# Performance work log

Measured on AMD Instinct MI355X. Metric: run time of the kernel, lower is better.

## Reference

```python
import jax, jax.numpy as jnp
import numpy as np

B, T, C, HS = 256, 512, 64, 64

def setup_inputs() -> dict:
    key = jax.random.key(0)
    k1, k2, k3, k4 = jax.random.split(key, 4)
    x = jax.random.normal(k1, (B, T, C), dtype=jnp.float32)
    # store Linear weights as [in, out] so projection is x @ W
    w_key = jax.random.normal(k2, (C, HS), dtype=jnp.float32) * (C ** -0.5)
    w_query = jax.random.normal(k3, (C, HS), dtype=jnp.float32) * (C ** -0.5)
    w_value = jax.random.normal(k4, (C, HS), dtype=jnp.float32) * (C ** -0.5)
    return {"x": x, "w_key": w_key, "w_query": w_query, "w_value": w_value}

def reference(x, w_key, w_query, w_value):
    Bx, Tx, Cx = x.shape
    k = x @ w_key              # [B,T,HS]
    q = x @ w_query            # [B,T,HS]
    v = x @ w_value            # [B,T,HS]
    # NOTE: original scales by C**-0.5 (input channel dim), not head_size**-0.5
    wei = jnp.einsum("btd,bsd->bts", q, k) * (Cx ** -0.5)  # [B,T,T]
    causal = jnp.tril(jnp.ones((Tx, Tx), dtype=bool))
    wei = jnp.where(causal, wei, -jnp.inf)
    wei = jax.nn.softmax(wei, axis=-1)
    # dropout p=0.0 -> identity
    out = jnp.einsum("bts,bsd->btd", wei, v)  # [B,T,HS]
    return out
```

## Files before the change

kernel.cpp:

```cpp
#include <hip/hip_runtime.h>


#define SEQ 512
#define CH  64

#define SLOT_STRIDE 72
#define SLOT_SIZE   (32 * SLOT_STRIDE)
#define WOFF        (8 * SLOT_SIZE)

typedef __attribute__((ext_vector_type(8))) short bf16x8;
typedef __attribute__((ext_vector_type(4))) short bf16x4;
typedef __attribute__((ext_vector_type(4))) float f32x4;

static __device__ __forceinline__ short f2bf(float f) {
  union { float f; unsigned u; } v; v.f = f;
  unsigned r = v.u + 0x7FFFu + ((v.u >> 16) & 1u);
  return (short)(r >> 16);
}

static __device__ __forceinline__ bf16x4 pack4(f32x4 v) {
  bf16x4 r;
  r[0] = f2bf(v[0]); r[1] = f2bf(v[1]); r[2] = f2bf(v[2]); r[3] = f2bf(v[3]);
  return r;
}

static __device__ __forceinline__ f32x4 mfma32(bf16x8 a, bf16x8 b, f32x4 c) {
  return __builtin_amdgcn_mfma_f32_16x16x32_bf16(a, b, c, 0, 0, 0);
}

static __device__ __forceinline__ unsigned pperm(float hi, float lo) {
#if defined(__has_builtin) && __has_builtin(__builtin_amdgcn_perm)
  return __builtin_amdgcn_perm(__builtin_bit_cast(unsigned, hi),
                               __builtin_bit_cast(unsigned, lo), 0x07060302u);
#else
  return (__builtin_bit_cast(unsigned, hi) & 0xFFFF0000u) |
         (__builtin_bit_cast(unsigned, lo) >> 16);
#endif
}

#if defined(__has_builtin) && __has_builtin(__builtin_amdgcn_exp2f)
#define EXP2(v) __builtin_amdgcn_exp2f(v)
#else
#define EXP2(v) __expf((v) * 0.6931471805599453f)
#endif

static __device__ __forceinline__ void wave_lds_fence() {
  asm volatile("s_waitcnt lgkmcnt(0)" ::: "memory");
}

static __device__ __forceinline__ void make_qf(
    const float* __restrict__ xb, const bf16x8 WQf[4][2],
    unsigned short* slot, int q0, int l15, int quad, bf16x8 qf[2][2]) {
#pragma unroll
  for (int nn = 0; nn < 2; ++nn) {
    bf16x8 xa[2];
#pragma unroll
    for (int c = 0; c < 2; ++c) {
      const float* px = xb + (size_t)(q0 + nn * 16 + l15) * CH + c * 32 + quad * 8;
      float4 lo = *(const float4*)px;
      float4 hi = *(const float4*)(px + 4);
      bf16x8 f;
      f[0] = f2bf(lo.x); f[1] = f2bf(lo.y); f[2] = f2bf(lo.z); f[3] = f2bf(lo.w);
      f[4] = f2bf(hi.x); f[5] = f2bf(hi.y); f[6] = f2bf(hi.z); f[7] = f2bf(hi.w);
      xa[c] = f;
    }
#pragma unroll
    for (int cht = 0; cht < 4; ++cht) {
      f32x4 qt = {0.f, 0.f, 0.f, 0.f};
#pragma unroll
      for (int c = 0; c < 2; ++c)
        qt = mfma32(WQf[cht][c], xa[c], qt);
      *(bf16x4*)(slot + (nn * 16 + l15) * SLOT_STRIDE + cht * 16 + quad * 4) = pack4(qt);
    }
  }
  wave_lds_fence();
#pragma unroll
  for (int nn = 0; nn < 2; ++nn)
#pragma unroll
    for (int c = 0; c < 2; ++c)
      qf[nn][c] = *(const bf16x8*)(slot + (nn * 16 + l15) * SLOT_STRIDE + c * 32 + quad * 8);
  wave_lds_fence();
}

static __device__ __forceinline__ void run_strip(
    int s, const bf16x8 qf[2][2], const unsigned short* __restrict__ ldsK,
    const unsigned short* __restrict__ ldsV, float* __restrict__ outb,
    int lane, int l15, int quad) {
  const int q0 = s * 32;
  f32x4 ot[2][4];
#pragma unroll
  for (int nn = 0; nn < 2; ++nn)
#pragma unroll
    for (int cht = 0; cht < 4; ++cht) ot[nn][cht] = (f32x4){0.f, 0.f, 0.f, 0.f};
  float ls0 = 0.f, ls1 = 0.f;
  const int dthr = l15 - quad * 4;

  bf16x8 kf[4];
#pragma unroll
  for (int i = 0; i < 4; ++i)
    kf[i] = *(const bf16x8*)(ldsK + i * 512 + lane * 8);

#pragma unroll 1
  for (int kt = 0; kt <= s; ++kt) {
    const bool diag = (kt == s);
    bf16x8 vf[4];
    const unsigned short* vp = ldsV + kt * 2048;
#pragma unroll
    for (int i = 0; i < 4; ++i)
      vf[i] = *(const bf16x8*)(vp + i * 512 + lane * 8);
    bf16x8 kn[4];
    if (!diag) {
      const unsigned short* kp = ldsK + (kt + 1) * 2048;
#pragma unroll
      for (int i = 0; i < 4; ++i)
        kn[i] = *(const bf16x8*)(kp + i * 512 + lane * 8);
    }

    f32x4 st00 = {0.f,0.f,0.f,0.f}, st01 = {0.f,0.f,0.f,0.f};
    f32x4 st10 = {0.f,0.f,0.f,0.f}, st11 = {0.f,0.f,0.f,0.f};
    st00 = mfma32(kf[0], qf[0][0], st00); st00 = mfma32(kf[1], qf[0][1], st00);
    st01 = mfma32(kf[0], qf[1][0], st01); st01 = mfma32(kf[1], qf[1][1], st01);
    st11 = mfma32(kf[2], qf[1][0], st11); st11 = mfma32(kf[3], qf[1][1], st11);
    if (!diag) {
      st10 = mfma32(kf[2], qf[0][0], st10); st10 = mfma32(kf[3], qf[0][1], st10);
    }

    union { bf16x8 v; unsigned u[4]; } P0, P1;
    if (diag) {
#pragma unroll
      for (int r = 0; r < 4; ++r) {
        st00[r] = (r > dthr) ? 0.f : EXP2(st00[r]);  ls0 += st00[r];
        st11[r] = (r > dthr) ? 0.f : EXP2(st11[r]);  ls1 += st11[r];
        st01[r] = EXP2(st01[r]);                     ls1 += st01[r];
      }
      P0.u[0] = pperm(st00[1], st00[0]); P0.u[1] = pperm(st00[3], st00[2]);
      P0.u[2] = 0u;                      P0.u[3] = 0u;
      P1.u[0] = pperm(st01[1], st01[0]); P1.u[1] = pperm(st01[3], st01[2]);
      P1.u[2] = pperm(st11[1], st11[0]); P1.u[3] = pperm(st11[3], st11[2]);
    } else {
#pragma unroll
      for (int r = 0; r < 4; ++r) {
        st00[r] = EXP2(st00[r]);  ls0 += st00[r];
        st10[r] = EXP2(st10[r]);  ls0 += st10[r];
        st01[r] = EXP2(st01[r]);  ls1 += st01[r];
        st11[r] = EXP2(st11[r]);  ls1 += st11[r];
      }
      P0.u[0] = pperm(st00[1], st00[0]); P0.u[1] = pperm(st00[3], st00[2]);
      P0.u[2] = pperm(st10[1], st10[0]); P0.u[3] = pperm(st10[3], st10[2]);
      P1.u[0] = pperm(st01[1], st01[0]); P1.u[1] = pperm(st01[3], st01[2]);
      P1.u[2] = pperm(st11[1], st11[0]); P1.u[3] = pperm(st11[3], st11[2]);
    }

    ot[0][0] = mfma32(vf[0], P0.v, ot[0][0]);  ot[1][0] = mfma32(vf[0], P1.v, ot[1][0]);
    ot[0][1] = mfma32(vf[1], P0.v, ot[0][1]);  ot[1][1] = mfma32(vf[1], P1.v, ot[1][1]);
    ot[0][2] = mfma32(vf[2], P0.v, ot[0][2]);  ot[1][2] = mfma32(vf[2], P1.v, ot[1][2]);
    ot[0][3] = mfma32(vf[3], P0.v, ot[0][3]);  ot[1][3] = mfma32(vf[3], P1.v, ot[1][3]);

    if (!diag) {
#pragma unroll
      for (int i = 0; i < 4; ++i) kf[i] = kn[i];
    }
  }

  ls0 += __shfl_xor(ls0, 16); ls0 += __shfl_xor(ls0, 32);
  ls1 += __shfl_xor(ls1, 16); ls1 += __shfl_xor(ls1, 32);
  const float inv0 = 1.0f / ls0, inv1 = 1.0f / ls1;

#pragma unroll
  for (int nn = 0; nn < 2; ++nn) {
    const float inv = nn ? inv1 : inv0;
#pragma unroll
    for (int cht = 0; cht < 4; ++cht) {
      float4 v;
      v.x = ot[nn][cht][0] * inv; v.y = ot[nn][cht][1] * inv;
      v.z = ot[nn][cht][2] * inv; v.w = ot[nn][cht][3] * inv;
      *(float4*)(outb + (size_t)(q0 + nn * 16 + l15) * CH + cht * 16 + quad * 4) = v;
    }
  }
}

__global__ __launch_bounds__(512, 2)
void attn_fused(const float* __restrict__ x,
                const float* __restrict__ wk,
                const float* __restrict__ wq,
                const float* __restrict__ wv,
                float* __restrict__ out) {
  __shared__ alignas(16) unsigned short ldsK[SEQ * CH];
  __shared__ alignas(16) unsigned short ldsV[SEQ * CH];

  const int b    = blockIdx.x;
  const int w    = threadIdx.x >> 6;
  const int lane = threadIdx.x & 63;
  const int l15  = lane & 15;
  const int quad = lane >> 4;

  const float* xb   = x + (size_t)b * SEQ * CH;
  float*       outb = out + (size_t)b * SEQ * CH;

  {
    const int t = w >> 1, c = w & 1;
    const int k0 = c * 32 + quad * 8;
    const int n  = t * 16 + l15;
#pragma unroll
    for (int m = 0; m < 3; ++m) {
      const float* Wsrc  = (m == 0) ? wq : (m == 1) ? wk : wv;
      const float  scale = (m == 0) ? 0.18033688011112042f : 1.0f;
      bf16x8 fr;
#pragma unroll
      for (int j = 0; j < 8; ++j)
        fr[j] = f2bf(Wsrc[(k0 + j) * CH + n] * scale);
      *(bf16x8*)(ldsK + WOFF + (m * 8 + w) * 512 + lane * 8) = fr;
    }
  }
  __syncthreads();

  const int sA = w, sB = 15 - w;
  unsigned short* slot = ldsK + w * SLOT_SIZE;
  bf16x8 qfA[2][2], qfB[2][2];
  {
    bf16x8 WQf[4][2];
#pragma unroll
    for (int t = 0; t < 4; ++t)
#pragma unroll
      for (int c = 0; c < 2; ++c)
        WQf[t][c] = *(const bf16x8*)(ldsK + WOFF + (t * 2 + c) * 512 + lane * 8);
    make_qf(xb, WQf, slot, sA * 32, l15, quad, qfA);
    make_qf(xb, WQf, slot, sB * 32, l15, quad, qfB);
  }

  {
    bf16x8 WKf[4][2], WVf[4][2];
#pragma unroll
    for (int t = 0; t < 4; ++t)
#pragma unroll
      for (int c = 0; c < 2; ++c) {
        WKf[t][c] = *(const bf16x8*)(ldsK + WOFF + (8  + t * 2 + c) * 512 + lane * 8);
        WVf[t][c] = *(const bf16x8*)(ldsK + WOFF + (16 + t * 2 + c) * 512 + lane * 8);
      }
    __syncthreads();

#pragma unroll
    for (int sub = 0; sub < 4; ++sub) {
      const int t16 = w * 64 + sub * 16;
      bf16x8 xa[2];
#pragma unroll
      for (int c = 0; c < 2; ++c) {
        const float* px = xb + (size_t)(t16 + l15) * CH + c * 32 + quad * 8;
        float4 lo = *(const float4*)px;
        float4 hi = *(const float4*)(px + 4);
        bf16x8 f;
        f[0] = f2bf(lo.x); f[1] = f2bf(lo.y); f[2] = f2bf(lo.z); f[3] = f2bf(lo.w);
        f[4] = f2bf(hi.x); f[5] = f2bf(hi.y); f[6] = f2bf(hi.z); f[7] = f2bf(hi.w);
        xa[c] = f;
      }
#pragma unroll
      for (int cht = 0; cht < 4; ++cht) {
        f32x4 ak = {0.f, 0.f, 0.f, 0.f};
#pragma unroll
        for (int c = 0; c < 2; ++c)
          ak = mfma32(WKf[cht][c], xa[c], ak);
        const int cdst = cht >> 1;
        const int qp   = ((cht & 1) << 1) | (quad >> 1);
        *(bf16x4*)(ldsK + (t16 >> 4) * 1024 + cdst * 512 +
                   (qp * 16 + l15) * 8 + (quad & 1) * 4) = pack4(ak);
      }
#pragma unroll
      for (int nt = 0; nt < 4; ++nt) {
        f32x4 av = {0.f, 0.f, 0.f, 0.f};
#pragma unroll
        for (int c = 0; c < 2; ++c)
          av = mfma32(xa[c], WVf[nt][c], av);
        *(bf16x4*)(ldsV + (t16 >> 5) * 2048 + nt * 512 +
                   (quad * 16 + l15) * 8 + ((t16 >> 4) & 1) * 4) = pack4(av);
      }
    }
  }
  __syncthreads();

  run_strip(sA, qfA, ldsK, ldsV, outb, lane, l15, quad);
  run_strip(sB, qfB, ldsK, ldsV, outb, lane, l15, quad);
}

extern "C" void kernel_launch(void* const* d_in, const int* in_sizes, int n_in,
                              void* d_out, int out_size, void* d_ws, size_t ws_size,
                              hipStream_t stream) {
  const float* x  = (const float*)d_in[0];
  const float* wk = (const float*)d_in[1];
  const float* wq = (const float*)d_in[2];
  const float* wv = (const float*)d_in[3];
  (void)in_sizes; (void)n_in; (void)out_size; (void)d_ws; (void)ws_size;
  attn_fused<<<256, 512, 0, stream>>>(x, wk, wq, wv, (float*)d_out);
}
```

Baseline: 99.91 us.

## Split attention into 16-row query strips across 16 waves per block

Doubles the block to 1024 threads (16 waves). Each wave now handles two balanced 16-row query strips (s and 31-s) instead of two 32-row strips, and K/V projection work is split across more waves. This raises per-block parallelism and latency hiding, and halves per-wave register state (one output accumulator set). The cost is that each K/V tile is reloaded from LDS by twice as many waves per query row, and the diagonal handling becomes an odd/even partial tile. The weight-staging loop is reworked to distribute 24 fragments over 16 waves.

```diff
diff --git a/kernel.cpp b/kernel.cpp
--- a/kernel.cpp
+++ b/kernel.cpp
@@ -5,8 +5,8 @@
 #define CH  64
 
 #define SLOT_STRIDE 72
-#define SLOT_SIZE   (32 * SLOT_STRIDE)
-#define WOFF        (8 * SLOT_SIZE)
+#define SLOT_SIZE   (16 * SLOT_STRIDE)
+#define WOFF        (16 * SLOT_SIZE)
 
 typedef __attribute__((ext_vector_type(8))) short bf16x8;
 typedef __attribute__((ext_vector_type(4))) short bf16x4;
@@ -48,51 +48,46 @@
   asm volatile("s_waitcnt lgkmcnt(0)" ::: "memory");
 }
 
-static __device__ __forceinline__ void make_qf(
+static __device__ __forceinline__ void make_qf16(
     const float* __restrict__ xb, const bf16x8 WQf[4][2],
-    unsigned short* slot, int q0, int l15, int quad, bf16x8 qf[2][2]) {
-#pragma unroll
-  for (int nn = 0; nn < 2; ++nn) {
-    bf16x8 xa[2];
-#pragma unroll
-    for (int c = 0; c < 2; ++c) {
-      const float* px = xb + (size_t)(q0 + nn * 16 + l15) * CH + c * 32 + quad * 8;
-      float4 lo = *(const float4*)px;
-      float4 hi = *(const float4*)(px + 4);
-      bf16x8 f;
-      f[0] = f2bf(lo.x); f[1] = f2bf(lo.y); f[2] = f2bf(lo.z); f[3] = f2bf(lo.w);
-      f[4] = f2bf(hi.x); f[5] = f2bf(hi.y); f[6] = f2bf(hi.z); f[7] = f2bf(hi.w);
-      xa[c] = f;
-    }
-#pragma unroll
-    for (int cht = 0; cht < 4; ++cht) {
-      f32x4 qt = {0.f, 0.f, 0.f, 0.f};
-#pragma unroll
-      for (int c = 0; c < 2; ++c)
-        qt = mfma32(WQf[cht][c], xa[c], qt);
-      *(bf16x4*)(slot + (nn * 16 + l15) * SLOT_STRIDE + cht * 16 + quad * 4) = pack4(qt);
-    }
+    unsigned short* slot, int q0, int l15, int quad, bf16x8 qf[2]) {
+  bf16x8 xa[2];
+#pragma unroll
+  for (int c = 0; c < 2; ++c) {
+    const float* px = xb + (size_t)(q0 + l15) * CH + c * 32 + quad * 8;
+    float4 lo = *(const float4*)px;
+    float4 hi = *(const float4*)(px + 4);
+    bf16x8 f;
+    f[0] = f2bf(lo.x); f[1] = f2bf(lo.y); f[2] = f2bf(lo.z); f[3] = f2bf(lo.w);
+    f[4] = f2bf(hi.x); f[5] = f2bf(hi.y); f[6] = f2bf(hi.z); f[7] = f2bf(hi.w);
+    xa[c] = f;
+  }
+#pragma unroll
+  for (int cht = 0; cht < 4; ++cht) {
+    f32x4 qt = {0.f, 0.f, 0.f, 0.f};
+#pragma unroll
+    for (int c = 0; c < 2; ++c)
+      qt = mfma32(WQf[cht][c], xa[c], qt);
+    *(bf16x4*)(slot + l15 * SLOT_STRIDE + cht * 16 + quad * 4) = pack4(qt);
   }
   wave_lds_fence();
 #pragma unroll
-  for (int nn = 0; nn < 2; ++nn)
-#pragma unroll
-    for (int c = 0; c < 2; ++c)
-      qf[nn][c] = *(const bf16x8*)(slot + (nn * 16 + l15) * SLOT_STRIDE + c * 32 + quad * 8);
+  for (int c = 0; c < 2; ++c)
+    qf[c] = *(const bf16x8*)(slot + l15 * SLOT_STRIDE + c * 32 + quad * 8);
   wave_lds_fence();
 }
 
-static __device__ __forceinline__ void run_strip(
-    int s, const bf16x8 qf[2][2], const unsigned short* __restrict__ ldsK,
+static __device__ __forceinline__ void run_strip16(
+    int s, const bf16x8 qf[2], const unsigned short* __restrict__ ldsK,
     const unsigned short* __restrict__ ldsV, float* __restrict__ outb,
     int lane, int l15, int quad) {
-  const int q0 = s * 32;
-  f32x4 ot[2][4];
-#pragma unroll
-  for (int nn = 0; nn < 2; ++nn)
-#pragma unroll
-    for (int cht = 0; cht < 4; ++cht) ot[nn][cht] = (f32x4){0.f, 0.f, 0.f, 0.f};
-  float ls0 = 0.f, ls1 = 0.f;
+  const int q0  = s * 16;
+  const int nd  = s >> 1;
+  const int odd = s & 1;
+  f32x4 ot[4];
+#pragma unroll
+  for (int cht = 0; cht < 4; ++cht) ot[cht] = (f32x4){0.f, 0.f, 0.f, 0.f};
+  float ls = 0.f;
   const int dthr = l15 - quad * 4;
 
   bf16x8 kf[4];
@@ -101,85 +96,85 @@
     kf[i] = *(const bf16x8*)(ldsK + i * 512 + lane * 8);
 
 #pragma unroll 1
-  for (int kt = 0; kt <= s; ++kt) {
-    const bool diag = (kt == s);
+  for (int t = 0; t < nd; ++t) {
+    bf16x8 vf[4], kn[4];
+    const unsigned short* vp = ldsV + t * 2048;
+    const unsigned short* kp = ldsK + (t + 1) * 2048;
+#pragma unroll
+    for (int i = 0; i < 4; ++i) {
+      vf[i] = *(const bf16x8*)(vp + i * 512 + lane * 8);
+      kn[i] = *(const bf16x8*)(kp + i * 512 + lane * 8);
+    }
+
+    f32x4 s0 = {0.f,0.f,0.f,0.f}, s1 = {0.f,0.f,0.f,0.f};
+    s0 = mfma32(kf[0], qf[0], s0); s0 = mfma32(kf[1], qf[1], s0);
+    s1 = mfma32(kf[2], qf[0], s1); s1 = mfma32(kf[3], qf[1], s1);
+
+    union { bf16x8 v; unsigned u[4]; } P;
+#pragma unroll
+    for (int r = 0; r < 4; ++r) {
+      s0[r] = EXP2(s0[r]);  ls += s0[r];
+      s1[r] = EXP2(s1[r]);  ls += s1[r];
+    }
+    P.u[0] = pperm(s0[1], s0[0]); P.u[1] = pperm(s0[3], s0[2]);
+    P.u[2] = pperm(s1[1], s1[0]); P.u[3] = pperm(s1[3], s1[2]);
+
+    ot[0] = mfma32(vf[0], P.v, ot[0]);
+    ot[1] = mfma32(vf[1], P.v, ot[1]);
+    ot[2] = mfma32(vf[2], P.v, ot[2]);
+    ot[3] = mfma32(vf[3], P.v, ot[3]);
+
+#pragma unroll
+    for (int i = 0; i < 4; ++i) kf[i] = kn[i];
+  }
+
+  {
     bf16x8 vf[4];
-    const unsigned short* vp = ldsV + kt * 2048;
+    const unsigned short* vp = ldsV + (size_t)nd * 2048;
 #pragma unroll
     for (int i = 0; i < 4; ++i)
       vf[i] = *(const bf16x8*)(vp + i * 512 + lane * 8);
-    bf16x8 kn[4];
-    if (!diag) {
-      const unsigned short* kp = ldsK + (kt + 1) * 2048;
-#pragma unroll
-      for (int i = 0; i < 4; ++i)
-        kn[i] = *(const bf16x8*)(kp + i * 512 + lane * 8);
-    }
-
-    f32x4 st00 = {0.f,0.f,0.f,0.f}, st01 = {0.f,0.f,0.f,0.f};
-    f32x4 st10 = {0.f,0.f,0.f,0.f}, st11 = {0.f,0.f,0.f,0.f};
-    st00 = mfma32(kf[0], qf[0][0], st00); st00 = mfma32(kf[1], qf[0][1], st00);
-    st01 = mfma32(kf[0], qf[1][0], st01); st01 = mfma32(kf[1], qf[1][1], st01);
-    st11 = mfma32(kf[2], qf[1][0], st11); st11 = mfma32(kf[3], qf[1][1], st11);
-    if (!diag) {
-      st10 = mfma32(kf[2], qf[0][0], st10); st10 = mfma32(kf[3], qf[0][1], st10);
-    }
-
-    union { bf16x8 v; unsigned u[4]; } P0, P1;
-    if (diag) {
+
+    f32x4 s0 = {0.f,0.f,0.f,0.f}, s1 = {0.f,0.f,0.f,0.f};
+    s0 = mfma32(kf[0], qf[0], s0); s0 = mfma32(kf[1], qf[1], s0);
+    if (odd) { s1 = mfma32(kf[2], qf[0], s1); s1 = mfma32(kf[3], qf[1], s1); }
+
+    union { bf16x8 v; unsigned u[4]; } P;
+    if (odd) {
 #pragma unroll
       for (int r = 0; r < 4; ++r) {
-        st00[r] = (r > dthr) ? 0.f : EXP2(st00[r]);  ls0 += st00[r];
-        st11[r] = (r > dthr) ? 0.f : EXP2(st11[r]);  ls1 += st11[r];
-        st01[r] = EXP2(st01[r]);                     ls1 += st01[r];
-      }
-      P0.u[0] = pperm(st00[1], st00[0]); P0.u[1] = pperm(st00[3], st00[2]);
-      P0.u[2] = 0u;                      P0.u[3] = 0u;
-      P1.u[0] = pperm(st01[1], st01[0]); P1.u[1] = pperm(st01[3], st01[2]);
-      P1.u[2] = pperm(st11[1], st11[0]); P1.u[3] = pperm(st11[3], st11[2]);
+        s0[r] = EXP2(s0[r]);                       ls += s0[r];
+        s1[r] = (r > dthr) ? 0.f : EXP2(s1[r]);    ls += s1[r];
+      }
+      P.u[0] = pperm(s0[1], s0[0]); P.u[1] = pperm(s0[3], s0[2]);
+      P.u[2] = pperm(s1[1], s1[0]); P.u[3] = pperm(s1[3], s1[2]);
     } else {
 #pragma unroll
       for (int r = 0; r < 4; ++r) {
-        st00[r] = EXP2(st00[r]);  ls0 += st00[r];
-        st10[r] = EXP2(st10[r]);  ls0 += st10[r];
-        st01[r] = EXP2(st01[r]);  ls1 += st01[r];
-        st11[r] = EXP2(st11[r]);  ls1 += st11[r];
-      }
-      P0.u[0] = pperm(st00[1], st00[0]); P0.u[1] = pperm(st00[3], st00[2]);
-      P0.u[2] = pperm(st10[1], st10[0]); P0.u[3] = pperm(st10[3], st10[2]);
-      P1.u[0] = pperm(st01[1], st01[0]); P1.u[1] = pperm(st01[3], st01[2]);
-      P1.u[2] = pperm(st11[1], st11[0]); P1.u[3] = pperm(st11[3], st11[2]);
-    }
-
-    ot[0][0] = mfma32(vf[0], P0.v, ot[0][0]);  ot[1][0] = mfma32(vf[0], P1.v, ot[1][0]);
-    ot[0][1] = mfma32(vf[1], P0.v, ot[0][1]);  ot[1][1] = mfma32(vf[1], P1.v, ot[1][1]);
-    ot[0][2] = mfma32(vf[2], P0.v, ot[0][2]);  ot[1][2] = mfma32(vf[2], P1.v, ot[1][2]);
-    ot[0][3] = mfma32(vf[3], P0.v, ot[0][3]);  ot[1][3] = mfma32(vf[3], P1.v, ot[1][3]);
-
-    if (!diag) {
-#pragma unroll
-      for (int i = 0; i < 4; ++i) kf[i] = kn[i];
-    }
-  }
-
-  ls0 += __shfl_xor(ls0, 16); ls0 += __shfl_xor(ls0, 32);
-  ls1 += __shfl_xor(ls1, 16); ls1 += __shfl_xor(ls1, 32);
-  const float inv0 = 1.0f / ls0, inv1 = 1.0f / ls1;
-
-#pragma unroll
-  for (int nn = 0; nn < 2; ++nn) {
-    const float inv = nn ? inv1 : inv0;
-#pragma unroll
-    for (int cht = 0; cht < 4; ++cht) {
-      float4 v;
-      v.x = ot[nn][cht][0] * inv; v.y = ot[nn][cht][1] * inv;
-      v.z = ot[nn][cht][2] * inv; v.w = ot[nn][cht][3] * inv;
-      *(float4*)(outb + (size_t)(q0 + nn * 16 + l15) * CH + cht * 16 + quad * 4) = v;
-    }
-  }
-}
-
-__global__ __launch_bounds__(512, 2)
+        s0[r] = (r > dthr) ? 0.f : EXP2(s0[r]);    ls += s0[r];
+      }
+      P.u[0] = pperm(s0[1], s0[0]); P.u[1] = pperm(s0[3], s0[2]);
+      P.u[2] = 0u; P.u[3] = 0u;
+    }
+    ot[0] = mfma32(vf[0], P.v, ot[0]);
+    ot[1] = mfma32(vf[1], P.v, ot[1]);
+    ot[2] = mfma32(vf[2], P.v, ot[2]);
+    ot[3] = mfma32(vf[3], P.v, ot[3]);
+  }
+
+  ls += __shfl_xor(ls, 16); ls += __shfl_xor(ls, 32);
+  const float inv = 1.0f / ls;
+
+#pragma unroll
+  for (int cht = 0; cht < 4; ++cht) {
+    float4 v;
+    v.x = ot[cht][0] * inv; v.y = ot[cht][1] * inv;
+    v.z = ot[cht][2] * inv; v.w = ot[cht][3] * inv;
+    *(float4*)(outb + (size_t)(q0 + l15) * CH + cht * 16 + quad * 4) = v;
+  }
+}
+
+__global__ __launch_bounds__(1024, 4)
 void attn_fused(const float* __restrict__ x,
                 const float* __restrict__ wk,
                 const float* __restrict__ wq,
@@ -198,25 +193,28 @@
   float*       outb = out + (size_t)b * SEQ * CH;
 
   {
-    const int t = w >> 1, c = w & 1;
-    const int k0 = c * 32 + quad * 8;
-    const int n  = t * 16 + l15;
-#pragma unroll
-    for (int m = 0; m < 3; ++m) {
+#pragma unroll
+    for (int pass = 0; pass < 2; ++pass) {
+      const int j = pass ? (16 + w) : w;
+      if (pass && w >= 8) break;
+      const int m  = j >> 3, wc = j & 7;
+      const int t  = wc >> 1, c = wc & 1;
+      const int k0 = c * 32 + quad * 8;
+      const int n  = t * 16 + l15;
       const float* Wsrc  = (m == 0) ? wq : (m == 1) ? wk : wv;
       const float  scale = (m == 0) ? 0.18033688011112042f : 1.0f;
       bf16x8 fr;
 #pragma unroll
-      for (int j = 0; j < 8; ++j)
-        fr[j] = f2bf(Wsrc[(k0 + j) * CH + n] * scale);
-      *(bf16x8*)(ldsK + WOFF + (m * 8 + w) * 512 + lane * 8) = fr;
+      for (int jj = 0; jj < 8; ++jj)
+        fr[jj] = f2bf(Wsrc[(k0 + jj) * CH + n] * scale);
+      *(bf16x8*)(ldsK + WOFF + (m * 8 + wc) * 512 + lane * 8) = fr;
     }
   }
   __syncthreads();
 
-  const int sA = w, sB = 15 - w;
+  const int sA = w, sB = 31 - w;
   unsigned short* slot = ldsK + w * SLOT_SIZE;
-  bf16x8 qfA[2][2], qfB[2][2];
+  bf16x8 qfA[2], qfB[2];
   {
     bf16x8 WQf[4][2];
 #pragma unroll
@@ -224,8 +222,8 @@
 #pragma unroll
       for (int c = 0; c < 2; ++c)
         WQf[t][c] = *(const bf16x8*)(ldsK + WOFF + (t * 2 + c) * 512 + lane * 8);
-    make_qf(xb, WQf, slot, sA * 32, l15, quad, qfA);
-    make_qf(xb, WQf, slot, sB * 32, l15, quad, qfB);
+    make_qf16(xb, WQf, slot, sA * 16, l15, quad, qfA);
+    make_qf16(xb, WQf, slot, sB * 16, l15, quad, qfB);
   }
 
   {
@@ -240,8 +238,8 @@
     __syncthreads();
 
 #pragma unroll
-    for (int sub = 0; sub < 4; ++sub) {
-      const int t16 = w * 64 + sub * 16;
+    for (int sub = 0; sub < 2; ++sub) {
+      const int t16 = w * 32 + sub * 16;
       bf16x8 xa[2];
 #pragma unroll
       for (int c = 0; c < 2; ++c) {
@@ -277,8 +275,8 @@
   }
   __syncthreads();
 
-  run_strip(sA, qfA, ldsK, ldsV, outb, lane, l15, quad);
-  run_strip(sB, qfB, ldsK, ldsV, outb, lane, l15, quad);
+  run_strip16(sA, qfA, ldsK, ldsV, outb, lane, l15, quad);
+  run_strip16(sB, qfB, ldsK, ldsV, outb, lane, l15, quad);
 }
 
 extern "C" void kernel_launch(void* const* d_in, const int* in_sizes, int n_in,
@@ -289,5 +287,5 @@
   const float* wq = (const float*)d_in[2];
   const float* wv = (const float*)d_in[3];
   (void)in_sizes; (void)n_in; (void)out_size; (void)d_ws; (void)ws_size;
-  attn_fused<<<256, 512, 0, stream>>>(x, wk, wq, wv, (float*)d_out);
-}
+  attn_fused<<<256, 1024, 0, stream>>>(x, wk, wq, wv, (float*)d_out);
+}
```

Measured after the change: 99.80 us. About the same (-0.1%).
